# Kernel tuning notes

Hardware: AMD Instinct MI355X
Metric: run time of the kernel (lower is better)

Reference implementation:

```python
import jax, jax.numpy as jnp
import numpy as np

NUM_HEADS = 4
HEAD_DIM = 64
BN_EPS = 1e-5


def setup_inputs() -> dict:
    key = jax.random.key(0)
    ks = jax.random.split(key, 6)
    B, C, H, W = 8, 256, 48, 48
    HD = NUM_HEADS * HEAD_DIM  # 256
    x = jax.random.normal(ks[0], (B, C, H, W), dtype=jnp.float32)
    q_w = jax.random.normal(ks[1], (HD, C), dtype=jnp.float32) * (1.0 / np.sqrt(C))
    k_w = jax.random.normal(ks[2], (HEAD_DIM, C), dtype=jnp.float32) * (1.0 / np.sqrt(C))
    v_w = jax.random.normal(ks[3], (HEAD_DIM, C), dtype=jnp.float32) * (1.0 / np.sqrt(C))
    proj_w = jax.random.normal(ks[4], (C, HD), dtype=jnp.float32) * (1.0 / np.sqrt(HD))
    proj_b = jnp.zeros((C,), dtype=jnp.float32)
    gamma = jnp.ones((C,), dtype=jnp.float32)
    beta = jnp.zeros((C,), dtype=jnp.float32)
    return {"x": x, "q_w": q_w, "k_w": k_w, "v_w": v_w,
            "proj_w": proj_w, "proj_b": proj_b, "gamma": gamma, "beta": beta}


def reference(x, q_w, k_w, v_w, proj_w, proj_b, gamma, beta):
    B, C, H, W = x.shape
    N = H * W
    scale = HEAD_DIM ** -0.5
    xf = x.reshape(B, C, N)  # 1x1 conv == channel matmul
    q = jnp.einsum('oc,bcn->bon', q_w, xf).reshape(B, NUM_HEADS, HEAD_DIM, N)
    k = jnp.einsum('dc,bcn->bdn', k_w, xf)  # shared single KV head (MQA)
    v = jnp.einsum('dc,bcn->bdn', v_w, xf)
    # scores: [B, heads, N, N]
    attn = jnp.einsum('bhdn,bdm->bhnm', q, k) * scale
    attn = jax.nn.softmax(attn, axis=-1)
    out = jnp.einsum('bhnm,bdm->bhdn', attn, v)  # [B, heads, d, N]
    out = out.reshape(B, NUM_HEADS * HEAD_DIM, N)
    out = jnp.einsum('co,bon->bcn', proj_w, out) + proj_b[None, :, None]
    out = out.reshape(B, C, H, W)
    # BatchNorm2d (training-mode batch statistics, biased variance)
    mean = jnp.mean(out, axis=(0, 2, 3), keepdims=True)
    var = jnp.var(out, axis=(0, 2, 3), keepdims=True)
    out = gamma[None, :, None, None] * (out - mean) * jax.lax.rsqrt(var + BN_EPS) + beta[None, :, None, None]
    return out + x
```

## Files before the change

### kernel.cpp

```cpp
#include <hip/hip_runtime.h>
#include <hip/hip_bf16.h>
#include <math.h>

#define BB 8
#define CCH 256
#define NN 2304
#define NH 4
#define HDIM 64
#define QKV_ROWS 384
#define BN_EPS 1e-5f
#define NTILES 36
#define HTILES 18
#define NPART 288
#define SLOG2E 0.18033688011112042f

typedef short bf16x8 __attribute__((ext_vector_type(8)));
typedef short bf16x4 __attribute__((ext_vector_type(4)));
typedef float f32x4 __attribute__((ext_vector_type(4)));

#if __has_builtin(__builtin_amdgcn_exp2f)
#define EXP2(x) __builtin_amdgcn_exp2f(x)
#else
#define EXP2(x) __expf((x) * 0.6931471805599453f)
#endif

#define MFMA16(a, b, c) __builtin_amdgcn_mfma_f32_16x16x16bf16_1k(a, b, c, 0, 0, 0)
#define MFMA32(a, b, c) __builtin_amdgcn_mfma_f32_16x16x32_bf16(a, b, c, 0, 0, 0)

__device__ __forceinline__ unsigned bfpair(float a, float b) {
    __hip_bfloat162 h = __float22bfloat162_rn(make_float2(a, b));
    return *(unsigned*)&h;
}
__device__ __forceinline__ unsigned short f2bf(float f) {
    unsigned u = __float_as_uint(f);
    u = (u + 0x7FFFu + ((u >> 16) & 1u)) >> 16;
    return (unsigned short)u;
}
__device__ __forceinline__ bf16x4 pack4(float p0, float p1, float p2, float p3) {
    union { unsigned u[2]; bf16x4 v; } x;
    x.u[0] = bfpair(p0, p1);
    x.u[1] = bfpair(p2, p3);
    return x.v;
}
__device__ __forceinline__ float bf2f(unsigned short s) {
    return __uint_as_float((unsigned)s << 16);
}

__global__ __launch_bounds__(256) void prep_k(
    const float* __restrict__ x,
    const float* __restrict__ qw, const float* __restrict__ kw,
    const float* __restrict__ vw, const float* __restrict__ pw,
    unsigned short* __restrict__ xT,
    unsigned short* __restrict__ Wb, unsigned short* __restrict__ Pb)
{
    const int bid = blockIdx.x;
    const int tid = threadIdx.x;
    if (bid < 1152) {
        __shared__ float sX[64][65];
        const int b  = bid / 144;
        const int rem = bid - b * 144;
        const int nb = (rem >> 2) * 64;
        const int cb = (rem & 3) * 64;

        #pragma unroll
        for (int u = 0; u < 4; ++u) {
            int c  = (tid >> 4) + 16 * u;
            int n4 = (tid & 15) * 4;
            float4 v = *(const float4*)(x + ((size_t)(b * CCH + cb + c)) * NN + nb + n4);
            sX[c][n4+0] = v.x; sX[c][n4+1] = v.y; sX[c][n4+2] = v.z; sX[c][n4+3] = v.w;
        }
        __syncthreads();

        const int n  = tid >> 2;
        const int cg = (tid & 3) * 16;
        unsigned vals[8];
        #pragma unroll
        for (int p = 0; p < 8; ++p)
            vals[p] = bfpair(sX[cg + 2*p][n], sX[cg + 2*p + 1][n]);
        unsigned short* dst = xT + ((size_t)(b * NN + nb + n)) * CCH + cb + cg;
        *(uint4*)dst = make_uint4(vals[0], vals[1], vals[2], vals[3]);
        *(uint4*)(dst + 8) = make_uint4(vals[4], vals[5], vals[6], vals[7]);
    } else {
        int idx = (bid - 1152) * 256 + tid;
        if (idx < 98304) {
            int o = idx >> 8, c = idx & 255;
            float v;
            if (o < 256)      v = qw[(size_t)o * CCH + c] * SLOG2E;
            else if (o < 320) v = kw[(size_t)(o - 256) * CCH + c];
            else              v = vw[(size_t)(o - 320) * CCH + c];
            Wb[idx] = f2bf(v);
        } else {
            int j = idx - 98304;
            if (j < 65536) Pb[j] = f2bf(pw[j]);
        }
    }
}

__global__ __launch_bounds__(128) void qkv_mfma_k(
    const unsigned short* __restrict__ Wb, const unsigned short* __restrict__ xT,
    unsigned short* __restrict__ Qt, unsigned short* __restrict__ Kt,
    unsigned short* __restrict__ Vn)
{
    __shared__ unsigned short sE[2][64 * 72];
    const int tid = threadIdx.x;
    const int wave = tid >> 6;
    const int lane = tid & 63;
    const int quad = lane >> 4;
    const int l15  = lane & 15;
    const int b  = blockIdx.x;
    const int nb = blockIdx.y * 64;
    const int mb = blockIdx.z * 128 + wave * 64;

    const unsigned short* Ab = Wb + (size_t)(mb + l15) * CCH + quad * 8;
    const unsigned short* Bb = xT + ((size_t)(b * NN + nb + l15)) * CCH + quad * 8;

    f32x4 C[4][4] = {};
    bf16x8 aA[2][4], bB[2][4];
    #pragma unroll
    for (int i = 0; i < 4; ++i) aA[0][i] = *(const bf16x8*)(Ab + (size_t)(16*i) * CCH);
    #pragma unroll
    for (int j = 0; j < 4; ++j) bB[0][j] = *(const bf16x8*)(Bb + (size_t)(16*j) * CCH);

    #pragma unroll
    for (int kk = 0; kk < 8; ++kk) {
        const int cur = kk & 1;
        if (kk < 7) {
            const int k1 = (kk + 1) * 32;
            #pragma unroll
            for (int i = 0; i < 4; ++i) aA[cur^1][i] = *(const bf16x8*)(Ab + (size_t)(16*i) * CCH + k1);
            #pragma unroll
            for (int j = 0; j < 4; ++j) bB[cur^1][j] = *(const bf16x8*)(Bb + (size_t)(16*j) * CCH + k1);
        }
        #pragma unroll
        for (int i = 0; i < 4; ++i)
            #pragma unroll
            for (int j = 0; j < 4; ++j)
                C[i][j] = MFMA32(aA[cur][i], bB[cur][j], C[i][j]);
    }

    unsigned short* sEw = &sE[wave][0];
    if (mb < 320) {
        #pragma unroll
        for (int i = 0; i < 4; ++i)
            #pragma unroll
            for (int j = 0; j < 4; ++j) {
                unsigned p01 = bfpair(C[i][j][0], C[i][j][1]);
                unsigned p23 = bfpair(C[i][j][2], C[i][j][3]);
                unsigned short* p = sEw + (16*j + l15) * 72 + 16*i + quad*4;
                *(unsigned*)p = p01;
                *(unsigned*)(p + 2) = p23;
            }
        if (mb < 256) {
            #pragma unroll
            for (int it = 0; it < 8; ++it) {
                int flat = lane + 64 * it;
                int row = flat >> 3;
                int o8  = (flat & 7) * 8;
                uint4 v = *(const uint4*)(sEw + row * 72 + o8);
                *(uint4*)(Qt + ((size_t)(b * NN + nb + row)) * CCH + mb + o8) = v;
            }
        } else {
            #pragma unroll
            for (int it = 0; it < 8; ++it) {
                int flat = lane + 64 * it;
                int row = flat >> 3;
                int o8  = (flat & 7) * 8;
                uint4 v = *(const uint4*)(sEw + row * 72 + o8);
                *(uint4*)(Kt + ((size_t)(b * NN + nb + row)) * 64 + o8) = v;
            }
        }
    } else {
        #pragma unroll
        for (int i = 0; i < 4; ++i)
            #pragma unroll
            for (int j = 0; j < 4; ++j) {
                unsigned p01 = bfpair(C[i][j][0], C[i][j][1]);
                unsigned p23 = bfpair(C[i][j][2], C[i][j][3]);
                unsigned short* p = sEw + (16*i + quad*4) * 72 + 16*j + l15;
                p[0]   = (unsigned short)p01;
                p[72]  = (unsigned short)(p01 >> 16);
                p[144] = (unsigned short)p23;
                p[216] = (unsigned short)(p23 >> 16);
            }
        #pragma unroll
        for (int it = 0; it < 8; ++it) {
            int flat = lane + 64 * it;
            int row = flat >> 3;
            int n8  = (flat & 7) * 8;
            uint4 v = *(const uint4*)(sEw + row * 72 + n8);
            *(uint4*)(Vn + ((size_t)(b * 64 + (mb - 320) + row)) * NN + nb + n8) = v;
        }
    }
}

__global__ __launch_bounds__(256, 4) void attn_k(
    const unsigned short* __restrict__ Qt,
    const unsigned short* __restrict__ Kt,
    const unsigned short* __restrict__ Vn,
    unsigned short* __restrict__ Ao)
{
    __shared__ __align__(16) unsigned short sKV[4 * 64 * 72];

    const int tid   = threadIdx.x;
    const int wave  = tid >> 6;
    const int lane  = tid & 63;
    const int quad  = lane >> 4;
    const int l15   = lane & 15;
    const int qslot = wave & 1;
    const int kh    = wave >> 1;
    const int qoff  = qslot * 32;
    const int b     = blockIdx.x;
    const int nb    = blockIdx.y * 64;
    const int head  = blockIdx.z;

    unsigned short* sKb = sKV + kh * 2 * 4608;
    unsigned short* sVb = sKb + 4608;

    bf16x8 bQ[2][2];
    const unsigned short* QtB = Qt + ((size_t)(b * NN + nb + qoff + l15)) * CCH + head * 64 + quad * 8;
    #pragma unroll
    for (int qt = 0; qt < 2; ++qt)
        #pragma unroll
        for (int s = 0; s < 2; ++s)
            bQ[qt][s] = *(const bf16x8*)(QtB + (size_t)(16*qt) * CCH + s * 32);

    bf16x8 pf[8];
    #pragma unroll
    for (int u = 0; u < 8; ++u) {
        const int buf   = u >> 1;
        const int khb   = buf >> 1;
        const int local = (u & 1) * 256 + tid;
        const int row   = local >> 3;
        const int ch8   = (local & 7) * 8;
        const int keys0 = khb * HTILES * 64;
        if ((buf & 1) == 0)
            pf[u] = *(const bf16x8*)(Kt + ((size_t)(b * NN + keys0 + row)) * 64 + ch8);
        else
            pf[u] = *(const bf16x8*)(Vn + ((size_t)(b * 64 + row)) * NN + keys0 + ch8);
    }

    f32x4 O[4][2] = {};
    float lacc[2] = {0.f, 0.f};

    for (int step = 0; step < HTILES; ++step) {
        __syncthreads();
        #pragma unroll
        for (int u = 0; u < 8; ++u) {
            const int buf   = u >> 1;
            const int local = (u & 1) * 256 + tid;
            const int row   = local >> 3;
            const int ch8   = (local & 7) * 8;
            *(bf16x8*)(sKV + buf * 4608 + row * 72 + ch8) = pf[u];
        }
        __syncthreads();

        if (step + 1 < HTILES) {
            #pragma unroll
            for (int u = 0; u < 8; ++u) {
                const int buf   = u >> 1;
                const int khb   = buf >> 1;
                const int local = (u & 1) * 256 + tid;
                const int row   = local >> 3;
                const int ch8   = (local & 7) * 8;
                const int keys0 = (khb * HTILES + step + 1) * 64;
                if ((buf & 1) == 0)
                    pf[u] = *(const bf16x8*)(Kt + ((size_t)(b * NN + keys0 + row)) * 64 + ch8);
                else
                    pf[u] = *(const bf16x8*)(Vn + ((size_t)(b * 64 + row)) * NN + keys0 + ch8);
            }
        }

        f32x4 C[4][2] = {};
        #pragma unroll
        for (int s = 0; s < 2; ++s)
            #pragma unroll
            for (int kt = 0; kt < 4; ++kt) {
                bf16x8 aK = *(const bf16x8*)(sKb + (16*kt + l15) * 72 + s * 32 + quad * 8);
                C[kt][0] = MFMA32(aK, bQ[0][s], C[kt][0]);
                C[kt][1] = MFMA32(aK, bQ[1][s], C[kt][1]);
            }

        bf16x4 bP[4][2];
        #pragma unroll
        for (int kt = 0; kt < 4; ++kt)
            #pragma unroll
            for (int qt = 0; qt < 2; ++qt) {
                float p0 = EXP2(C[kt][qt][0]);
                float p1 = EXP2(C[kt][qt][1]);
                float p2 = EXP2(C[kt][qt][2]);
                float p3 = EXP2(C[kt][qt][3]);
                lacc[qt] += (p0 + p1) + (p2 + p3);
                bP[kt][qt] = pack4(p0, p1, p2, p3);
            }

        #pragma unroll
        for (int jd = 0; jd < 4; ++jd)
            #pragma unroll
            for (int kt = 0; kt < 4; ++kt) {
                bf16x4 aV = *(const bf16x4*)(sVb + (16*jd + l15) * 72 + 16*kt + quad*4);
                O[jd][0] = MFMA16(aV, bP[kt][0], O[jd][0]);
                O[jd][1] = MFMA16(aV, bP[kt][1], O[jd][1]);
            }
    }
    __syncthreads();

    float* sc = (float*)sKV;
    unsigned short* sT = (unsigned short*)sKV + 9216;
    if (kh == 1) {
        const int base = qslot * 2304 + lane * 36;
        #pragma unroll
        for (int jd = 0; jd < 4; ++jd)
            #pragma unroll
            for (int qt = 0; qt < 2; ++qt)
                *(f32x4*)(sc + base + jd * 8 + qt * 4) = O[jd][qt];
        sc[base + 32] = lacc[0];
        sc[base + 33] = lacc[1];
    }
    __syncthreads();
    if (kh == 0) {
        const int base = qslot * 2304 + lane * 36;
        #pragma unroll
        for (int jd = 0; jd < 4; ++jd)
            #pragma unroll
            for (int qt = 0; qt < 2; ++qt)
                O[jd][qt] += *(const f32x4*)(sc + base + jd * 8 + qt * 4);
        lacc[0] += sc[base + 32];
        lacc[1] += sc[base + 33];

        float rinv[2];
        #pragma unroll
        for (int qt = 0; qt < 2; ++qt) {
            float s = lacc[qt];
            s += __shfl_xor(s, 16);
            s += __shfl_xor(s, 32);
            rinv[qt] = 1.0f / s;
        }
        #pragma unroll
        for (int qt = 0; qt < 2; ++qt)
            #pragma unroll
            for (int jd = 0; jd < 4; ++jd) {
                unsigned lo = bfpair(O[jd][qt][0] * rinv[qt], O[jd][qt][1] * rinv[qt]);
                unsigned hi = bfpair(O[jd][qt][2] * rinv[qt], O[jd][qt][3] * rinv[qt]);
                *(uint2*)(sT + (qoff + 16*qt + l15) * 72 + 16*jd + quad*4) = make_uint2(lo, hi);
            }
    }
    __syncthreads();

    #pragma unroll
    for (int it = 0; it < 2; ++it) {
        int flat = tid + 256 * it;
        int row = flat >> 3;
        int c8  = (flat & 7) * 8;
        uint4 v = *(const uint4*)(sT + row * 72 + c8);
        *(uint4*)(Ao + ((size_t)(b * NN + nb + row)) * CCH + head * 64 + c8) = v;
    }
}

__global__ __launch_bounds__(128) void proj_mfma_k(
    const unsigned short* __restrict__ Pb, const unsigned short* __restrict__ Ao,
    const float* __restrict__ pb, unsigned short* __restrict__ projb,
    float* __restrict__ psum, float* __restrict__ psq)
{
    __shared__ unsigned short sE[2][64 * 72];
    const int tid = threadIdx.x;
    const int wave = tid >> 6;
    const int lane = tid & 63;
    const int quad = lane >> 4;
    const int l15  = lane & 15;
    const int b  = blockIdx.x;
    const int nb = blockIdx.y * 64;
    const int mb = blockIdx.z * 128 + wave * 64;
    const int part = b * NTILES + blockIdx.y;

    const unsigned short* Ab = Pb + (size_t)(mb + l15) * CCH + quad * 8;
    const unsigned short* Bb = Ao + ((size_t)(b * NN + nb + l15)) * CCH + quad * 8;

    f32x4 C[4][4] = {};
    bf16x8 aA[2][4], bB[2][4];
    #pragma unroll
    for (int i = 0; i < 4; ++i) aA[0][i] = *(const bf16x8*)(Ab + (size_t)(16*i) * CCH);
    #pragma unroll
    for (int j = 0; j < 4; ++j) bB[0][j] = *(const bf16x8*)(Bb + (size_t)(16*j) * CCH);

    #pragma unroll
    for (int kk = 0; kk < 8; ++kk) {
        const int cur = kk & 1;
        if (kk < 7) {
            const int k1 = (kk + 1) * 32;
            #pragma unroll
            for (int i = 0; i < 4; ++i) aA[cur^1][i] = *(const bf16x8*)(Ab + (size_t)(16*i) * CCH + k1);
            #pragma unroll
            for (int j = 0; j < 4; ++j) bB[cur^1][j] = *(const bf16x8*)(Bb + (size_t)(16*j) * CCH + k1);
        }
        #pragma unroll
        for (int i = 0; i < 4; ++i)
            #pragma unroll
            for (int j = 0; j < 4; ++j)
                C[i][j] = MFMA32(aA[cur][i], bB[cur][j], C[i][j]);
    }

    unsigned short* sEw = &sE[wave][0];
    #pragma unroll
    for (int i = 0; i < 4; ++i) {
        #pragma unroll
        for (int r = 0; r < 4; ++r) {
            const int ch = mb + 16*i + quad*4 + r;
            const float bias = pb[ch];
            float v0 = C[i][0][r] + bias, v1 = C[i][1][r] + bias;
            float v2 = C[i][2][r] + bias, v3 = C[i][3][r] + bias;
            C[i][0][r] = v0; C[i][1][r] = v1; C[i][2][r] = v2; C[i][3][r] = v3;
            float rs = (v0 + v1) + (v2 + v3);
            float rq = (v0*v0 + v1*v1) + (v2*v2 + v3*v3);
            rs += __shfl_xor(rs, 1); rq += __shfl_xor(rq, 1);
            rs += __shfl_xor(rs, 2); rq += __shfl_xor(rq, 2);
            rs += __shfl_xor(rs, 4); rq += __shfl_xor(rq, 4);
            rs += __shfl_xor(rs, 8); rq += __shfl_xor(rq, 8);
            if (l15 == 0) {
                psum[(size_t)ch * NPART + part] = rs;
                psq [(size_t)ch * NPART + part] = rq;
            }
        }
    }

    #pragma unroll
    for (int i = 0; i < 4; ++i)
        #pragma unroll
        for (int j = 0; j < 4; ++j) {
            unsigned p01 = bfpair(C[i][j][0], C[i][j][1]);
            unsigned p23 = bfpair(C[i][j][2], C[i][j][3]);
            unsigned short* p = sEw + (16*i + quad*4) * 72 + 16*j + l15;
            p[0]   = (unsigned short)p01;
            p[72]  = (unsigned short)(p01 >> 16);
            p[144] = (unsigned short)p23;
            p[216] = (unsigned short)(p23 >> 16);
        }
    #pragma unroll
    for (int it = 0; it < 8; ++it) {
        int flat = lane + 64 * it;
        int row = flat >> 3;
        int n8  = (flat & 7) * 8;
        uint4 v = *(const uint4*)(sEw + row * 72 + n8);
        *(uint4*)(projb + ((size_t)(b * CCH + mb + row)) * NN + nb + n8) = v;
    }
}

__global__ __launch_bounds__(64) void bn_finalize_k(
    const float* __restrict__ psum, const float* __restrict__ psq,
    const float* __restrict__ gamma, const float* __restrict__ beta,
    float* __restrict__ stats)
{
    const int c = blockIdx.x;
    const int lane = threadIdx.x;
    float s = 0.f, q = 0.f;
    for (int k = lane; k < NPART; k += 64) {
        s += psum[(size_t)c * NPART + k];
        q += psq [(size_t)c * NPART + k];
    }
    #pragma unroll
    for (int off = 1; off < 64; off <<= 1) {
        s += __shfl_xor(s, off);
        q += __shfl_xor(q, off);
    }
    if (lane == 0) {
        const float inv_n = 1.0f / (float)(BB * NN);
        float mean = s * inv_n;
        float var  = q * inv_n - mean * mean;
        float sc = gamma[c] * rsqrtf(var + BN_EPS);
        stats[c] = sc;
        stats[CCH + c] = beta[c] - mean * sc;
    }
}

__global__ __launch_bounds__(256) void bn_apply_k(
    const unsigned short* __restrict__ projb, const float* __restrict__ x,
    const float* __restrict__ stats, float* __restrict__ out)
{
    size_t idx = ((size_t)blockIdx.x * 256 + threadIdx.x) * 8;
    const size_t total = (size_t)BB * CCH * NN;
    if (idx >= total) return;
    int c = (int)((idx / NN) % CCH);
    float sc = stats[c], sh = stats[CCH + c];
    uint4 pv = *(const uint4*)(projb + idx);
    const unsigned short* ps = (const unsigned short*)&pv;
    float4 x0 = *(const float4*)(x + idx);
    float4 x1 = *(const float4*)(x + idx + 4);
    float4 r0, r1;
    r0.x = sc * bf2f(ps[0]) + sh + x0.x;
    r0.y = sc * bf2f(ps[1]) + sh + x0.y;
    r0.z = sc * bf2f(ps[2]) + sh + x0.z;
    r0.w = sc * bf2f(ps[3]) + sh + x0.w;
    r1.x = sc * bf2f(ps[4]) + sh + x1.x;
    r1.y = sc * bf2f(ps[5]) + sh + x1.y;
    r1.z = sc * bf2f(ps[6]) + sh + x1.z;
    r1.w = sc * bf2f(ps[7]) + sh + x1.w;
    *(float4*)(out + idx) = r0;
    *(float4*)(out + idx + 4) = r1;
}

extern "C" void kernel_launch(void* const* d_in, const int* in_sizes, int n_in,
                              void* d_out, int out_size, void* d_ws, size_t ws_size,
                              hipStream_t stream)
{
    const float* x     = (const float*)d_in[0];
    const float* qw    = (const float*)d_in[1];
    const float* kw    = (const float*)d_in[2];
    const float* vw    = (const float*)d_in[3];
    const float* pw    = (const float*)d_in[4];
    const float* pb    = (const float*)d_in[5];
    const float* gamma = (const float*)d_in[6];
    const float* beta  = (const float*)d_in[7];
    float* out = (float*)d_out;

    char* ws = (char*)d_ws;
    unsigned short* xT = (unsigned short*)ws;
    unsigned short* Ao = (unsigned short*)ws;
    unsigned short* Wb = (unsigned short*)(ws + 9437184);
    unsigned short* Pb = (unsigned short*)(ws + 9633792);
    unsigned short* Qt = (unsigned short*)(ws + 9764864);
    unsigned short* Kt = (unsigned short*)(ws + 19202048);
    unsigned short* Vn = (unsigned short*)(ws + 21561344);
    unsigned short* projb = (unsigned short*)(ws + 9764864);
    float* stats = (float*)(ws + 28639232);
    float* psum  = (float*)(ws + 28641280);
    float* psq   = (float*)(ws + 28936192);

    prep_k<<<1792, 256, 0, stream>>>(x, qw, kw, vw, pw, xT, Wb, Pb);

    dim3 g1(BB, NN / 64, 3);
    qkv_mfma_k<<<g1, 128, 0, stream>>>(Wb, xT, Qt, Kt, Vn);

    dim3 g2(BB, NN / 64, NH);
    attn_k<<<g2, 256, 0, stream>>>(Qt, Kt, Vn, Ao);

    dim3 g3(BB, NN / 64, 2);
    proj_mfma_k<<<g3, 128, 0, stream>>>(Pb, Ao, pb, projb, psum, psq);

    bn_finalize_k<<<CCH, 64, 0, stream>>>(psum, psq, gamma, beta, stats);

    int total8 = BB * CCH * NN / 8;
    bn_apply_k<<<(total8 + 255) / 256, 256, 0, stream>>>(projb, x, stats, out);
}
```

Before: 200.2 us.

## Share MQA K/V tiles across two heads and shrink projection GEMM tiles

```diff
diff --git a/kernel.cpp b/kernel.cpp
--- a/kernel.cpp
+++ b/kernel.cpp
@@ -11,7 +11,7 @@
 #define BN_EPS 1e-5f
 #define NTILES 36
 #define HTILES 18
-#define NPART 288
+#define NPART 576
 #define SLOG2E 0.18033688011112042f
 
 typedef short bf16x8 __attribute__((ext_vector_type(8)));
@@ -101,25 +101,25 @@
     unsigned short* __restrict__ Qt, unsigned short* __restrict__ Kt,
     unsigned short* __restrict__ Vn)
 {
-    __shared__ unsigned short sE[2][64 * 72];
+    __shared__ unsigned short sE[2][64 * 40];
     const int tid = threadIdx.x;
     const int wave = tid >> 6;
     const int lane = tid & 63;
     const int quad = lane >> 4;
     const int l15  = lane & 15;
     const int b  = blockIdx.x;
-    const int nb = blockIdx.y * 64;
+    const int nb = blockIdx.y * 32;
     const int mb = blockIdx.z * 128 + wave * 64;
 
     const unsigned short* Ab = Wb + (size_t)(mb + l15) * CCH + quad * 8;
     const unsigned short* Bb = xT + ((size_t)(b * NN + nb + l15)) * CCH + quad * 8;
 
-    f32x4 C[4][4] = {};
-    bf16x8 aA[2][4], bB[2][4];
+    f32x4 C[4][2] = {};
+    bf16x8 aA[2][4], bB[2][2];
     #pragma unroll
     for (int i = 0; i < 4; ++i) aA[0][i] = *(const bf16x8*)(Ab + (size_t)(16*i) * CCH);
     #pragma unroll
-    for (int j = 0; j < 4; ++j) bB[0][j] = *(const bf16x8*)(Bb + (size_t)(16*j) * CCH);
+    for (int j = 0; j < 2; ++j) bB[0][j] = *(const bf16x8*)(Bb + (size_t)(16*j) * CCH);
 
     #pragma unroll
     for (int kk = 0; kk < 8; ++kk) {
@@ -129,12 +129,12 @@
             #pragma unroll
             for (int i = 0; i < 4; ++i) aA[cur^1][i] = *(const bf16x8*)(Ab + (size_t)(16*i) * CCH + k1);
             #pragma unroll
-            for (int j = 0; j < 4; ++j) bB[cur^1][j] = *(const bf16x8*)(Bb + (size_t)(16*j) * CCH + k1);
+            for (int j = 0; j < 2; ++j) bB[cur^1][j] = *(const bf16x8*)(Bb + (size_t)(16*j) * CCH + k1);
         }
         #pragma unroll
         for (int i = 0; i < 4; ++i)
             #pragma unroll
-            for (int j = 0; j < 4; ++j)
+            for (int j = 0; j < 2; ++j)
                 C[i][j] = MFMA32(aA[cur][i], bB[cur][j], C[i][j]);
     }
 
@@ -143,7 +143,7 @@
         #pragma unroll
         for (int i = 0; i < 4; ++i)
             #pragma unroll
-            for (int j = 0; j < 4; ++j) {
+            for (int j = 0; j < 2; ++j) {
                 unsigned p01 = bfpair(C[i][j][0], C[i][j][1]);
                 unsigned p23 = bfpair(C[i][j][2], C[i][j][3]);
                 unsigned short* p = sEw + (16*j + l15) * 72 + 16*i + quad*4;
@@ -152,7 +152,7 @@
             }
         if (mb < 256) {
             #pragma unroll
-            for (int it = 0; it < 8; ++it) {
+            for (int it = 0; it < 4; ++it) {
                 int flat = lane + 64 * it;
                 int row = flat >> 3;
                 int o8  = (flat & 7) * 8;
@@ -161,7 +161,7 @@
             }
         } else {
             #pragma unroll
-            for (int it = 0; it < 8; ++it) {
+            for (int it = 0; it < 4; ++it) {
                 int flat = lane + 64 * it;
                 int row = flat >> 3;
                 int o8  = (flat & 7) * 8;
@@ -173,27 +173,27 @@
         #pragma unroll
         for (int i = 0; i < 4; ++i)
             #pragma unroll
-            for (int j = 0; j < 4; ++j) {
+            for (int j = 0; j < 2; ++j) {
                 unsigned p01 = bfpair(C[i][j][0], C[i][j][1]);
                 unsigned p23 = bfpair(C[i][j][2], C[i][j][3]);
-                unsigned short* p = sEw + (16*i + quad*4) * 72 + 16*j + l15;
+                unsigned short* p = sEw + (16*i + quad*4) * 40 + 16*j + l15;
                 p[0]   = (unsigned short)p01;
-                p[72]  = (unsigned short)(p01 >> 16);
-                p[144] = (unsigned short)p23;
-                p[216] = (unsigned short)(p23 >> 16);
-            }
-        #pragma unroll
-        for (int it = 0; it < 8; ++it) {
+                p[40]  = (unsigned short)(p01 >> 16);
+                p[80]  = (unsigned short)p23;
+                p[120] = (unsigned short)(p23 >> 16);
+            }
+        #pragma unroll
+        for (int it = 0; it < 4; ++it) {
             int flat = lane + 64 * it;
-            int row = flat >> 3;
-            int n8  = (flat & 7) * 8;
-            uint4 v = *(const uint4*)(sEw + row * 72 + n8);
+            int row = flat >> 2;
+            int n8  = (flat & 3) * 8;
+            uint4 v = *(const uint4*)(sEw + row * 40 + n8);
             *(uint4*)(Vn + ((size_t)(b * 64 + (mb - 320) + row)) * NN + nb + n8) = v;
         }
     }
 }
 
-__global__ __launch_bounds__(256, 4) void attn_k(
+__global__ __launch_bounds__(512, 4) void attn_k(
     const unsigned short* __restrict__ Qt,
     const unsigned short* __restrict__ Kt,
     const unsigned short* __restrict__ Vn,
@@ -207,15 +207,18 @@
     const int quad  = lane >> 4;
     const int l15   = lane & 15;
     const int qslot = wave & 1;
-    const int kh    = wave >> 1;
+    const int kh    = (wave >> 1) & 1;
+    const int hloc  = wave >> 2;
     const int qoff  = qslot * 32;
     const int b     = blockIdx.x;
     const int nb    = blockIdx.y * 64;
-    const int head  = blockIdx.z;
+    const int head  = blockIdx.z * 2 + hloc;
 
     unsigned short* sKb = sKV + kh * 2 * 4608;
     unsigned short* sVb = sKb + 4608;
 
+    const bf16x4 vone = {(short)0x3F80, (short)0x3F80, (short)0x3F80, (short)0x3F80};
+
     bf16x8 bQ[2][2];
     const unsigned short* QtB = Qt + ((size_t)(b * NN + nb + qoff + l15)) * CCH + head * 64 + quad * 8;
     #pragma unroll
@@ -224,49 +227,36 @@
         for (int s = 0; s < 2; ++s)
             bQ[qt][s] = *(const bf16x8*)(QtB + (size_t)(16*qt) * CCH + s * 32);
 
-    bf16x8 pf[8];
-    #pragma unroll
-    for (int u = 0; u < 8; ++u) {
-        const int buf   = u >> 1;
-        const int khb   = buf >> 1;
-        const int local = (u & 1) * 256 + tid;
-        const int row   = local >> 3;
-        const int ch8   = (local & 7) * 8;
-        const int keys0 = khb * HTILES * 64;
-        if ((buf & 1) == 0)
-            pf[u] = *(const bf16x8*)(Kt + ((size_t)(b * NN + keys0 + row)) * 64 + ch8);
+    const int srow = tid >> 3;
+    const int sch8 = (tid & 7) * 8;
+    bf16x8 pf[4];
+    #pragma unroll
+    for (int u = 0; u < 4; ++u) {
+        const int keys0 = (u >> 1) * HTILES * 64;
+        if ((u & 1) == 0)
+            pf[u] = *(const bf16x8*)(Kt + ((size_t)(b * NN + keys0 + srow)) * 64 + sch8);
         else
-            pf[u] = *(const bf16x8*)(Vn + ((size_t)(b * 64 + row)) * NN + keys0 + ch8);
+            pf[u] = *(const bf16x8*)(Vn + ((size_t)(b * 64 + srow)) * NN + keys0 + sch8);
     }
 
     f32x4 O[4][2] = {};
-    float lacc[2] = {0.f, 0.f};
+    f32x4 dacc[2] = {};
 
     for (int step = 0; step < HTILES; ++step) {
         __syncthreads();
         #pragma unroll
-        for (int u = 0; u < 8; ++u) {
-            const int buf   = u >> 1;
-            const int local = (u & 1) * 256 + tid;
-            const int row   = local >> 3;
-            const int ch8   = (local & 7) * 8;
-            *(bf16x8*)(sKV + buf * 4608 + row * 72 + ch8) = pf[u];
-        }
+        for (int u = 0; u < 4; ++u)
+            *(bf16x8*)(sKV + u * 4608 + srow * 72 + sch8) = pf[u];
         __syncthreads();
 
         if (step + 1 < HTILES) {
             #pragma unroll
-            for (int u = 0; u < 8; ++u) {
-                const int buf   = u >> 1;
-                const int khb   = buf >> 1;
-                const int local = (u & 1) * 256 + tid;
-                const int row   = local >> 3;
-                const int ch8   = (local & 7) * 8;
-                const int keys0 = (khb * HTILES + step + 1) * 64;
-                if ((buf & 1) == 0)
-                    pf[u] = *(const bf16x8*)(Kt + ((size_t)(b * NN + keys0 + row)) * 64 + ch8);
+            for (int u = 0; u < 4; ++u) {
+                const int keys0 = ((u >> 1) * HTILES + step + 1) * 64;
+                if ((u & 1) == 0)
+                    pf[u] = *(const bf16x8*)(Kt + ((size_t)(b * NN + keys0 + srow)) * 64 + sch8);
                 else
-                    pf[u] = *(const bf16x8*)(Vn + ((size_t)(b * 64 + row)) * NN + keys0 + ch8);
+                    pf[u] = *(const bf16x8*)(Vn + ((size_t)(b * 64 + srow)) * NN + keys0 + sch8);
             }
         }
 
@@ -284,14 +274,15 @@
         #pragma unroll
         for (int kt = 0; kt < 4; ++kt)
             #pragma unroll
-            for (int qt = 0; qt < 2; ++qt) {
-                float p0 = EXP2(C[kt][qt][0]);
-                float p1 = EXP2(C[kt][qt][1]);
-                float p2 = EXP2(C[kt][qt][2]);
-                float p3 = EXP2(C[kt][qt][3]);
-                lacc[qt] += (p0 + p1) + (p2 + p3);
-                bP[kt][qt] = pack4(p0, p1, p2, p3);
-            }
+            for (int qt = 0; qt < 2; ++qt)
+                bP[kt][qt] = pack4(EXP2(C[kt][qt][0]), EXP2(C[kt][qt][1]),
+                                   EXP2(C[kt][qt][2]), EXP2(C[kt][qt][3]));
+
+        #pragma unroll
+        for (int kt = 0; kt < 4; ++kt) {
+            dacc[0] = MFMA16(vone, bP[kt][0], dacc[0]);
+            dacc[1] = MFMA16(vone, bP[kt][1], dacc[1]);
+        }
 
         #pragma unroll
         for (int jd = 0; jd < 4; ++jd)
@@ -305,54 +296,50 @@
     __syncthreads();
 
     float* sc = (float*)sKV;
-    unsigned short* sT = (unsigned short*)sKV + 9216;
+    const int base = (hloc * 2 + qslot) * 2304 + lane * 36;
     if (kh == 1) {
-        const int base = qslot * 2304 + lane * 36;
         #pragma unroll
         for (int jd = 0; jd < 4; ++jd)
             #pragma unroll
             for (int qt = 0; qt < 2; ++qt)
                 *(f32x4*)(sc + base + jd * 8 + qt * 4) = O[jd][qt];
-        sc[base + 32] = lacc[0];
-        sc[base + 33] = lacc[1];
+        sc[base + 32] = dacc[0][0];
+        sc[base + 33] = dacc[1][0];
     }
     __syncthreads();
+    float rinv[2] = {0.f, 0.f};
     if (kh == 0) {
-        const int base = qslot * 2304 + lane * 36;
         #pragma unroll
         for (int jd = 0; jd < 4; ++jd)
             #pragma unroll
             for (int qt = 0; qt < 2; ++qt)
                 O[jd][qt] += *(const f32x4*)(sc + base + jd * 8 + qt * 4);
-        lacc[0] += sc[base + 32];
-        lacc[1] += sc[base + 33];
-
-        float rinv[2];
-        #pragma unroll
-        for (int qt = 0; qt < 2; ++qt) {
-            float s = lacc[qt];
-            s += __shfl_xor(s, 16);
-            s += __shfl_xor(s, 32);
-            rinv[qt] = 1.0f / s;
-        }
+        rinv[0] = 1.0f / (dacc[0][0] + sc[base + 32]);
+        rinv[1] = 1.0f / (dacc[1][0] + sc[base + 33]);
+    }
+    __syncthreads();
+
+    unsigned short* sT = (unsigned short*)sKV;
+    if (kh == 0) {
         #pragma unroll
         for (int qt = 0; qt < 2; ++qt)
             #pragma unroll
             for (int jd = 0; jd < 4; ++jd) {
                 unsigned lo = bfpair(O[jd][qt][0] * rinv[qt], O[jd][qt][1] * rinv[qt]);
                 unsigned hi = bfpair(O[jd][qt][2] * rinv[qt], O[jd][qt][3] * rinv[qt]);
-                *(uint2*)(sT + (qoff + 16*qt + l15) * 72 + 16*jd + quad*4) = make_uint2(lo, hi);
+                *(uint2*)(sT + (hloc * 64 + qoff + 16*qt + l15) * 72 + 16*jd + quad*4) = make_uint2(lo, hi);
             }
     }
     __syncthreads();
 
     #pragma unroll
     for (int it = 0; it < 2; ++it) {
-        int flat = tid + 256 * it;
-        int row = flat >> 3;
-        int c8  = (flat & 7) * 8;
-        uint4 v = *(const uint4*)(sT + row * 72 + c8);
-        *(uint4*)(Ao + ((size_t)(b * NN + nb + row)) * CCH + head * 64 + c8) = v;
+        int flat = tid + 512 * it;
+        int hh   = flat >> 9;
+        int row  = (flat >> 3) & 63;
+        int c8   = (flat & 7) * 8;
+        uint4 v = *(const uint4*)(sT + (hh * 64 + row) * 72 + c8);
+        *(uint4*)(Ao + ((size_t)(b * NN + nb + row)) * CCH + (blockIdx.z * 2 + hh) * 64 + c8) = v;
     }
 }
 
@@ -361,26 +348,26 @@
     const float* __restrict__ pb, unsigned short* __restrict__ projb,
     float* __restrict__ psum, float* __restrict__ psq)
 {
-    __shared__ unsigned short sE[2][64 * 72];
+    __shared__ unsigned short sE[2][64 * 40];
     const int tid = threadIdx.x;
     const int wave = tid >> 6;
     const int lane = tid & 63;
     const int quad = lane >> 4;
     const int l15  = lane & 15;
     const int b  = blockIdx.x;
-    const int nb = blockIdx.y * 64;
+    const int nb = blockIdx.y * 32;
     const int mb = blockIdx.z * 128 + wave * 64;
-    const int part = b * NTILES + blockIdx.y;
+    const int part = b * 72 + blockIdx.y;
 
     const unsigned short* Ab = Pb + (size_t)(mb + l15) * CCH + quad * 8;
     const unsigned short* Bb = Ao + ((size_t)(b * NN + nb + l15)) * CCH + quad * 8;
 
-    f32x4 C[4][4] = {};
-    bf16x8 aA[2][4], bB[2][4];
+    f32x4 C[4][2] = {};
+    bf16x8 aA[2][4], bB[2][2];
     #pragma unroll
     for (int i = 0; i < 4; ++i) aA[0][i] = *(const bf16x8*)(Ab + (size_t)(16*i) * CCH);
     #pragma unroll
-    for (int j = 0; j < 4; ++j) bB[0][j] = *(const bf16x8*)(Bb + (size_t)(16*j) * CCH);
+    for (int j = 0; j < 2; ++j) bB[0][j] = *(const bf16x8*)(Bb + (size_t)(16*j) * CCH);
 
     #pragma unroll
     for (int kk = 0; kk < 8; ++kk) {
@@ -390,12 +377,12 @@
             #pragma unroll
             for (int i = 0; i < 4; ++i) aA[cur^1][i] = *(const bf16x8*)(Ab + (size_t)(16*i) * CCH + k1);
             #pragma unroll
-            for (int j = 0; j < 4; ++j) bB[cur^1][j] = *(const bf16x8*)(Bb + (size_t)(16*j) * CCH + k1);
+            for (int j = 0; j < 2; ++j) bB[cur^1][j] = *(const bf16x8*)(Bb + (size_t)(16*j) * CCH + k1);
         }
         #pragma unroll
         for (int i = 0; i < 4; ++i)
             #pragma unroll
-            for (int j = 0; j < 4; ++j)
+            for (int j = 0; j < 2; ++j)
                 C[i][j] = MFMA32(aA[cur][i], bB[cur][j], C[i][j]);
     }
 
@@ -407,10 +394,9 @@
             const int ch = mb + 16*i + quad*4 + r;
             const float bias = pb[ch];
             float v0 = C[i][0][r] + bias, v1 = C[i][1][r] + bias;
-            float v2 = C[i][2][r] + bias, v3 = C[i][3][r] + bias;
-            C[i][0][r] = v0; C[i][1][r] = v1; C[i][2][r] = v2; C[i][3][r] = v3;
-            float rs = (v0 + v1) + (v2 + v3);
-            float rq = (v0*v0 + v1*v1) + (v2*v2 + v3*v3);
+            C[i][0][r] = v0; C[i][1][r] = v1;
+            float rs = v0 + v1;
+            float rq = v0*v0 + v1*v1;
             rs += __shfl_xor(rs, 1); rq += __shfl_xor(rq, 1);
             rs += __shfl_xor(rs, 2); rq += __shfl_xor(rq, 2);
             rs += __shfl_xor(rs, 4); rq += __shfl_xor(rq, 4);
@@ -425,21 +411,21 @@
     #pragma unroll
     for (int i = 0; i < 4; ++i)
         #pragma unroll
-        for (int j = 0; j < 4; ++j) {
+        for (int j = 0; j < 2; ++j) {
             unsigned p01 = bfpair(C[i][j][0], C[i][j][1]);
             unsigned p23 = bfpair(C[i][j][2], C[i][j][3]);
-            unsigned short* p = sEw + (16*i + quad*4) * 72 + 16*j + l15;
+            unsigned short* p = sEw + (16*i + quad*4) * 40 + 16*j + l15;
             p[0]   = (unsigned short)p01;
-            p[72]  = (unsigned short)(p01 >> 16);
-            p[144] = (unsigned short)p23;
-            p[216] = (unsigned short)(p23 >> 16);
-        }
-    #pragma unroll
-    for (int it = 0; it < 8; ++it) {
+            p[40]  = (unsigned short)(p01 >> 16);
+            p[80]  = (unsigned short)p23;
+            p[120] = (unsigned short)(p23 >> 16);
+        }
+    #pragma unroll
+    for (int it = 0; it < 4; ++it) {
         int flat = lane + 64 * it;
-        int row = flat >> 3;
-        int n8  = (flat & 7) * 8;
-        uint4 v = *(const uint4*)(sEw + row * 72 + n8);
+        int row = flat >> 2;
+        int n8  = (flat & 3) * 8;
+        uint4 v = *(const uint4*)(sEw + row * 40 + n8);
         *(uint4*)(projb + ((size_t)(b * CCH + mb + row)) * NN + nb + n8) = v;
     }
 }
@@ -522,17 +508,17 @@
     unsigned short* projb = (unsigned short*)(ws + 9764864);
     float* stats = (float*)(ws + 28639232);
     float* psum  = (float*)(ws + 28641280);
-    float* psq   = (float*)(ws + 28936192);
+    float* psq   = (float*)(ws + 29231104);
 
     prep_k<<<1792, 256, 0, stream>>>(x, qw, kw, vw, pw, xT, Wb, Pb);
 
-    dim3 g1(BB, NN / 64, 3);
+    dim3 g1(BB, 72, 3);
     qkv_mfma_k<<<g1, 128, 0, stream>>>(Wb, xT, Qt, Kt, Vn);
 
-    dim3 g2(BB, NN / 64, NH);
-    attn_k<<<g2, 256, 0, stream>>>(Qt, Kt, Vn, Ao);
-
-    dim3 g3(BB, NN / 64, 2);
+    dim3 g2(BB, NN / 64, NH / 2);
+    attn_k<<<g2, 512, 0, stream>>>(Qt, Kt, Vn, Ao);
+
+    dim3 g3(BB, 72, 2);
     proj_mfma_k<<<g3, 128, 0, stream>>>(Pb, Ao, pb, projb, psum, psq);
 
     bn_finalize_k<<<CCH, 64, 0, stream>>>(psum, psq, gamma, beta, stats);
```

Result: slower. 208.9 us (+4.4%).
